# Kernel tuning notes

Hardware: AMD Instinct MI355X
Metric: run time of the kernel (lower is better)

## Reference

```python
import jax, jax.numpy as jnp
import numpy as np

NUM_SLOTS = 7
DIM = 4096
NUM_HEADS = 8
HEAD_DIM = DIM // NUM_HEADS
LN_EPS = 1e-5


def setup_inputs() -> dict:
    key = jax.random.key(0)
    ks = jax.random.split(key, 9)
    B, N = 8, 2048
    x = jax.random.normal(ks[0], (B, N, DIM), dtype=jnp.float32)
    slots = 1e-4 * jax.random.normal(ks[1], (NUM_SLOTS, DIM), dtype=jnp.float32)
    ln_g = jnp.ones((DIM,), jnp.float32)
    ln_b = jnp.zeros((DIM,), jnp.float32)
    # nn.MultiheadAttention packed in-projection: rows [Wq; Wk; Wv], each (DIM, DIM)
    s = 1.0 / np.sqrt(DIM)
    in_proj_w = jax.random.uniform(ks[2], (3 * DIM, DIM), jnp.float32, -s, s)
    in_proj_b = jnp.zeros((3 * DIM,), jnp.float32)
    out_proj_w = jax.random.uniform(ks[3], (DIM, DIM), jnp.float32, -s, s)
    out_proj_b = jnp.zeros((DIM,), jnp.float32)
    alpha = 0.1 * jax.random.normal(ks[4], (1,), jnp.float32)  # nonzero so gate path is active
    return {"x": x, "slots": slots, "ln_g": ln_g, "ln_b": ln_b,
            "in_proj_w": in_proj_w, "in_proj_b": in_proj_b,
            "out_proj_w": out_proj_w, "out_proj_b": out_proj_b, "alpha": alpha}


def _cmrm(x, slots, ln_g, ln_b, in_proj_w, in_proj_b, out_proj_w, out_proj_b, alpha):
    x32 = x.astype(jnp.float32)
    # pre LayerNorm
    mu = jnp.mean(x32, axis=-1, keepdims=True)
    var = jnp.mean(jnp.square(x32 - mu), axis=-1, keepdims=True)
    xn = (x32 - mu) * jax.lax.rsqrt(var + LN_EPS) * ln_g + ln_b  # (B,N,D)
    slots_c = jnp.clip(slots, -10.0, 10.0)  # (Q,D), Q=7
    Wq, Wk, Wv = jnp.split(in_proj_w, 3, axis=0)
    bq, bk, bv = jnp.split(in_proj_b, 3, axis=0)
    q = slots_c @ Wq.T + bq                      # (Q,D), identical for all batches
    k = xn @ Wk.T + bk                           # (B,N,D)
    v = xn @ Wv.T + bv                           # (B,N,D)
    B, N, _ = x.shape
    qh = q.reshape(NUM_SLOTS, NUM_HEADS, HEAD_DIM)          # (Q,H,hd)
    kh = k.reshape(B, N, NUM_HEADS, HEAD_DIM)
    vh = v.reshape(B, N, NUM_HEADS, HEAD_DIM)
    scale = 1.0 / np.sqrt(HEAD_DIM)
    scores = jnp.einsum('qhd,bnhd->bhqn', qh * scale, kh)   # (B,H,Q,N)
    attn = jax.nn.softmax(scores, axis=-1)
    ctx = jnp.einsum('bhqn,bnhd->bqhd', attn, vh).reshape(B, NUM_SLOTS, DIM)
    slots_out = ctx @ out_proj_w.T + out_proj_b             # (B,Q,D)
    slots_res = slots_c[None] + slots_out                   # residual, ungated slots
    gate = jnp.tanh(alpha)                                  # (1,)
    g = jnp.mean(gate * slots_res, axis=1, keepdims=True)   # (B,1,D)
    x_refined = (x32 + g).astype(x.dtype)
    attn_weights = jnp.mean(attn, axis=1)                   # torch avg over heads -> (B,Q,N)
    return x_refined, attn_weights


def reference(x, slots, ln_g, ln_b, in_proj_w, in_proj_b, out_proj_w, out_proj_b, alpha):
    return _cmrm(x, slots, ln_g, ln_b, in_proj_w, in_proj_b, out_proj_w, out_proj_b, alpha)
```

## Files before the change

kernel.cpp:

```cpp
#include <hip/hip_runtime.h>

typedef __attribute__((ext_vector_type(4))) float f32x4;
typedef __attribute__((ext_vector_type(8))) short short8x;

#define DIM   4096
#define NB    8
#define NN    2048
#define NROWS (NB*NN)
#define NHD   8
#define NQ    7
#define NHQ   56
#define SCALE 0.04419417382415922f

#define OFF_MU     0L
#define OFF_RSTD   16384L
#define OFF_Q7     32768L
#define OFF_A      61440L
#define OFF_D0     61504L
#define OFF_S1     61568L
#define OFF_SMST   61632L
#define OFF_CTXM   62528L
#define OFF_GFIN   95296L
#define OFF_YM     128064L
#define OFF_UGBF   390208L
#define OFF_STATP  521280L
#define OFF_SCT    652352L
#define OFF_BIG    1700928L
#define OFF_AM     (OFF_BIG)
#define OFF_PART   (OFF_BIG + 131072L)

__device__ __forceinline__ unsigned short f2bf(float f) {
  union { float f; unsigned int u; } v; v.f = f;
  return (unsigned short)((v.u + 0x7FFFu + ((v.u >> 16) & 1u)) >> 16);
}
__device__ __forceinline__ unsigned short f2bfr(float f) {
  union { float f; unsigned int u; } v; v.f = f;
  return (unsigned short)((v.u + 0x8000u) >> 16);
}

__device__ __forceinline__ float waveSum(float v) {
  #pragma unroll
  for (int m = 1; m < 64; m <<= 1) v += __shfl_xor(v, m);
  return v;
}
__device__ __forceinline__ float blockSum256(float v, float* red) {
  v = waveSum(v);
  __syncthreads();
  if ((threadIdx.x & 63) == 0) red[threadIdx.x >> 6] = v;
  __syncthreads();
  return red[0] + red[1] + red[2] + red[3];
}
__device__ __forceinline__ float blockMax256(float v, float* red) {
  #pragma unroll
  for (int m = 1; m < 64; m <<= 1) v = fmaxf(v, __shfl_xor(v, m));
  __syncthreads();
  if ((threadIdx.x & 63) == 0) red[threadIdx.x >> 6] = v;
  __syncthreads();
  return fmaxf(fmaxf(red[0], red[1]), fmaxf(red[2], red[3]));
}

__global__ __launch_bounds__(256) void k_qproj(const float* __restrict__ ipw,
    const float* __restrict__ ipb, const float* __restrict__ slots, float* __restrict__ q7) {
  const int w = threadIdx.x >> 6, l = threadIdx.x & 63;
  const int d = blockIdx.x * 4 + w;
  const float4* wr4 = (const float4*)(ipw + (long)d * DIM);
  float acc[7] = {0,0,0,0,0,0,0};
  for (int e4 = l; e4 < 1024; e4 += 64) {
    float4 wv = wr4[e4];
    #pragma unroll
    for (int s = 0; s < 7; s++) {
      float4 sv = ((const float4*)(slots + (long)s*DIM))[e4];
      sv.x = fminf(fmaxf(sv.x, -10.f), 10.f); sv.y = fminf(fmaxf(sv.y, -10.f), 10.f);
      sv.z = fminf(fmaxf(sv.z, -10.f), 10.f); sv.w = fminf(fmaxf(sv.w, -10.f), 10.f);
      acc[s] += wv.x*sv.x + wv.y*sv.y + wv.z*sv.z + wv.w*sv.w;
    }
  }
  #pragma unroll
  for (int s = 0; s < 7; s++) acc[s] = waveSum(acc[s]);
  if (l == 0) {
    float bq = ipb[d];
    #pragma unroll
    for (int s = 0; s < 7; s++) q7[(long)s*DIM + d] = acc[s] + bq;
  }
}

__global__ __launch_bounds__(64) void k_adinit(const float* __restrict__ q7,
    const float* __restrict__ ipb, float* __restrict__ Aarr, float* __restrict__ D0arr) {
  const int hq = blockIdx.x, h = hq / 7, q = hq % 7;
  float acc = 0;
  for (int i = threadIdx.x; i < 512; i += 64)
    acc += q7[(long)q*DIM + h*512 + i] * ipb[DIM + h*512 + i];
  acc = waveSum(acc);
  if (threadIdx.x == 0) { Aarr[hq] = 0.f; D0arr[hq] = SCALE * acc; }
}

__global__ __launch_bounds__(256) void k_uproj(const float* __restrict__ ipw,
    const float* __restrict__ q7, float* __restrict__ upart) {
  const int h = blockIdx.y, c = blockIdx.z;
  const int e = blockIdx.x * 256 + threadIdx.x;
  __shared__ float qs[7][128];
  for (int i = threadIdx.x; i < 7*128; i += 256) {
    int s = i >> 7, hd = i & 127;
    qs[s][hd] = q7[(long)s*DIM + h*512 + c*128 + hd];
  }
  __syncthreads();
  float acc[7] = {0,0,0,0,0,0,0};
  const float* wp = ipw + ((long)(DIM + h*512 + c*128))*DIM + e;
  for (int hd = 0; hd < 128; hd++) {
    float wv = wp[(long)hd * DIM];
    #pragma unroll
    for (int s = 0; s < 7; s++) acc[s] += qs[s][hd] * wv;
  }
  #pragma unroll
  for (int s = 0; s < 7; s++) upart[(long)((c*8 + h)*7 + s)*DIM + e] = acc[s];
}

__global__ __launch_bounds__(256) void k_ured(const float* __restrict__ upart,
    const float* __restrict__ lng, const float* __restrict__ lnb,
    unsigned short* __restrict__ ugbf, float* __restrict__ Aarr, float* __restrict__ D0arr) {
  const int h = blockIdx.y;
  const int e = blockIdx.x * 256 + threadIdx.x;
  if (h == 8) {
    #pragma unroll
    for (int r = 0; r < 8; r++) ugbf[(long)(56 + r)*DIM + e] = 0;
    return;
  }
  float ge = lng[e], be = lnb[e];
  #pragma unroll
  for (int s = 0; s < 7; s++) {
    float u = 0;
    #pragma unroll
    for (int c = 0; c < 4; c++) u += upart[(long)((c*8 + h)*7 + s)*DIM + e];
    u *= SCALE;
    ugbf[(long)(h*7 + s)*DIM + e] = f2bf(u * ge);
    float pa = waveSum(u * ge);
    float pd = waveSum(u * be);
    if ((threadIdx.x & 63) == 0) {
      atomicAdd(&Aarr[h*7 + s], pa);
      atomicAdd(&D0arr[h*7 + s], pd);
    }
  }
}

__global__ __launch_bounds__(256) void k_scores2(const float* __restrict__ x,
    const unsigned short* __restrict__ ugbf, float* __restrict__ raw, float2* __restrict__ statp) {
  const int tid = threadIdx.x;
  const int w = tid >> 6, l = tid & 63;
  const int lr = l & 15, lk8 = (l >> 4) * 8;
  const int rowblk = blockIdx.x >> 2, ks = blockIdx.x & 3;
  const int row0w = rowblk * 64 + w * 16;
  const long arow = (long)(row0w + lr) * DIM;
  const int kbase = ks * 1024;
  f32x4 acc0 = {0,0,0,0}, acc1 = {0,0,0,0}, acc2 = {0,0,0,0}, acc3 = {0,0,0,0};
  float sx = 0.f, sxx = 0.f;
  const long b0 = (long)(0*16 + lr)*DIM, b1 = (long)(1*16 + lr)*DIM,
             b2 = (long)(2*16 + lr)*DIM, b3 = (long)(3*16 + lr)*DIM;
  #pragma unroll 2
  for (int kc = kbase; kc < kbase + 1024; kc += 32) {
    const float4 v0 = *(const float4*)(x + arow + kc + lk8);
    const float4 v1 = *(const float4*)(x + arow + kc + lk8 + 4);
    sx  += (v0.x + v0.y) + (v0.z + v0.w) + (v1.x + v1.y) + (v1.z + v1.w);
    sxx += v0.x*v0.x + v0.y*v0.y + v0.z*v0.z + v0.w*v0.w
         + v1.x*v1.x + v1.y*v1.y + v1.z*v1.z + v1.w*v1.w;
    short8x a;
    a[0] = (short)f2bfr(v0.x); a[1] = (short)f2bfr(v0.y);
    a[2] = (short)f2bfr(v0.z); a[3] = (short)f2bfr(v0.w);
    a[4] = (short)f2bfr(v1.x); a[5] = (short)f2bfr(v1.y);
    a[6] = (short)f2bfr(v1.z); a[7] = (short)f2bfr(v1.w);
    short8x bb0 = *(const short8x*)(ugbf + b0 + kc + lk8);
    acc0 = __builtin_amdgcn_mfma_f32_16x16x32_bf16(a, bb0, acc0, 0, 0, 0);
    short8x bb1 = *(const short8x*)(ugbf + b1 + kc + lk8);
    acc1 = __builtin_amdgcn_mfma_f32_16x16x32_bf16(a, bb1, acc1, 0, 0, 0);
    short8x bb2 = *(const short8x*)(ugbf + b2 + kc + lk8);
    acc2 = __builtin_amdgcn_mfma_f32_16x16x32_bf16(a, bb2, acc2, 0, 0, 0);
    short8x bb3 = *(const short8x*)(ugbf + b3 + kc + lk8);
    acc3 = __builtin_amdgcn_mfma_f32_16x16x32_bf16(a, bb3, acc3, 0, 0, 0);
  }
  sx += __shfl_xor(sx, 16);  sx += __shfl_xor(sx, 32);
  sxx += __shfl_xor(sxx, 16); sxx += __shfl_xor(sxx, 32);
  if (l < 16) {
    float2 p; p.x = sx; p.y = sxx;
    statp[(long)ks*NROWS + row0w + l] = p;
  }
  const long base = ((long)ks*NROWS + row0w) * 64;
  #pragma unroll
  for (int i = 0; i < 4; i++) {
    long ro = base + (long)((l >> 4)*4 + i) * 64 + lr;
    raw[ro +  0] = acc0[i];
    raw[ro + 16] = acc1[i];
    raw[ro + 32] = acc2[i];
    raw[ro + 48] = acc3[i];
  }
}

__global__ __launch_bounds__(256) void k_sepi(const float* __restrict__ raw,
    const float2* __restrict__ statp, const float* __restrict__ Aarr,
    const float* __restrict__ D0arr, float* __restrict__ mu_o, float* __restrict__ rstd_o,
    float* __restrict__ sct) {
  const int w = threadIdx.x >> 6, l = threadIdx.x & 63;
  const int row = blockIdx.x * 4 + w;
  float s = 0;
  #pragma unroll
  for (int ks = 0; ks < 4; ks++) s += raw[((long)ks*NROWS + row)*64 + l];
  float sx = 0, sxx = 0;
  #pragma unroll
  for (int ks = 0; ks < 4; ks++) {
    float2 p = statp[(long)ks*NROWS + row];
    sx += p.x; sxx += p.y;
  }
  float mu = sx * (1.0f/DIM), var = sxx * (1.0f/DIM) - mu*mu;
  float rs = rsqrtf(var + 1e-5f);
  if (l == 0) { mu_o[row] = mu; rstd_o[row] = rs; }
  if (l < NHQ) sct[(long)l*NROWS + row] = rs*(s - mu*Aarr[l]) + D0arr[l];
}

__global__ __launch_bounds__(256) void k_smax(const float* __restrict__ sct,
    float2* __restrict__ stats, float* __restrict__ s1) {
  __shared__ float red[4];
  if (blockIdx.x == 0 && threadIdx.x < 64) s1[threadIdx.x] = 0.f;
  const int b = blockIdx.x / NHQ, hq = blockIdx.x % NHQ;
  const int tid = threadIdx.x;
  const float* sp = sct + (long)hq*NROWS + (long)b*NN;
  float s[8]; float mx = -3.4e38f;
  #pragma unroll
  for (int j = 0; j < 8; j++) { s[j] = sp[tid + j*256]; mx = fmaxf(mx, s[j]); }
  mx = blockMax256(mx, red);
  float sum = 0;
  #pragma unroll
  for (int j = 0; j < 8; j++) sum += __expf(s[j] - mx);
  sum = blockSum256(sum, red);
  if (tid == 0) { float2 o; o.x = mx; o.y = 1.0f/sum; stats[b*NHQ + hq] = o; }
}

__global__ __launch_bounds__(256) void k_attnmeans(const float* __restrict__ sct,
    const float2* __restrict__ stats, const float* __restrict__ mu, const float* __restrict__ rstd,
    float* __restrict__ am, float* __restrict__ s1, float* __restrict__ out_attn) {
  const int b = blockIdx.x >> 3, nc = blockIdx.x & 7;
  const int tid = threadIdx.x;
  const int n = nc*256 + tid, row = b*NN + n;
  __shared__ float2 st[56];
  if (tid < 56) st[tid] = stats[b*NHQ + tid];
  __syncthreads();
  const float mur = mu[row] * rstd[row];
  float aq[7] = {0,0,0,0,0,0,0};
  #pragma unroll
  for (int h = 0; h < 8; h++) {
    float ah = 0;
    #pragma unroll
    for (int q = 0; q < 7; q++) {
      float2 s2 = st[h*7 + q];
      float p = __expf(sct[(long)(h*7 + q)*NROWS + row] - s2.x) * s2.y;
      aq[q] += p; ah += p;
    }
    float amv = ah * (1.0f/7.0f);
    am[((long)(b*8 + h))*NN + n] = amv;
    float sv = waveSum(amv * mur);
    if ((tid & 63) == 0) atomicAdd(&s1[b*8 + h], sv);
  }
  #pragma unroll
  for (int q = 0; q < 7; q++) out_attn[((long)(b*NQ + q))*NN + n] = aq[q] * 0.125f;
}

__global__ __launch_bounds__(256) void k_ypart(const float* __restrict__ x,
    const float* __restrict__ am, const float* __restrict__ rstd, float* __restrict__ part) {
  const int bid = blockIdx.x;
  const int b = bid >> 7, ec = (bid >> 5) & 3, nc = bid & 31;
  __shared__ float amr[8][64];
  const int tid = threadIdx.x;
  for (int i = tid; i < 512; i += 256) {
    int h = i >> 6, nn = i & 63;
    int row = b*NN + nc*64 + nn;
    amr[h][nn] = am[((long)(b*8 + h))*NN + nc*64 + nn] * rstd[row];
  }
  __syncthreads();
  const int e = ec*1024 + tid*4;
  float ax[8], ay[8], az[8], aw[8];
  #pragma unroll
  for (int h = 0; h < 8; h++) { ax[h]=0; ay[h]=0; az[h]=0; aw[h]=0; }
  const float* xp = x + ((long)(b*NN + nc*64))*DIM + e;
  #pragma unroll 2
  for (int nn = 0; nn < 64; nn++) {
    const float4 xv = *(const float4*)(xp + (long)nn*DIM);
    #pragma unroll
    for (int h = 0; h < 8; h++) {
      float a = amr[h][nn];
      ax[h] += a*xv.x; ay[h] += a*xv.y; az[h] += a*xv.z; aw[h] += a*xv.w;
    }
  }
  #pragma unroll
  for (int h = 0; h < 8; h++) {
    float4 o; o.x = ax[h]; o.y = ay[h]; o.z = az[h]; o.w = aw[h];
    *(float4*)&part[((long)(nc*64 + b*8 + h))*DIM + e] = o;
  }
}

__global__ __launch_bounds__(256) void k_yred(const float* __restrict__ part,
    const float* __restrict__ s1, const float* __restrict__ lng, const float* __restrict__ lnb,
    float* __restrict__ ym) {
  const long i4 = (long)blockIdx.x*256 + threadIdx.x;
  const float4* p4 = (const float4*)part;
  float4 s = p4[i4];
  #pragma unroll
  for (int nc = 1; nc < 32; nc++) {
    float4 v = p4[(long)nc*65536 + i4];
    s.x += v.x; s.y += v.y; s.z += v.z; s.w += v.w;
  }
  const int bh = (int)(i4 >> 10), e4 = (int)(i4 & 1023);
  float sv = s1[bh];
  float4 g = ((const float4*)lng)[e4], bb = ((const float4*)lnb)[e4];
  float4 o;
  o.x = g.x*(s.x - sv) + bb.x; o.y = g.y*(s.y - sv) + bb.y;
  o.z = g.z*(s.z - sv) + bb.z; o.w = g.w*(s.w - sv) + bb.w;
  ((float4*)ym)[i4] = o;
}

__global__ __launch_bounds__(256) void k_ctxm(const float* __restrict__ ipw,
    const float* __restrict__ ipb, const float* __restrict__ ym, float* __restrict__ ctxm) {
  const int w = threadIdx.x >> 6, l = threadIdx.x & 63;
  const int d = blockIdx.x*4 + w;
  const int h = d >> 9;
  const float4* wr4 = (const float4*)(ipw + ((long)(2*DIM + d))*DIM);
  float acc[8] = {0,0,0,0,0,0,0,0};
  for (int e4 = l; e4 < 1024; e4 += 64) {
    float4 wv = wr4[e4];
    #pragma unroll
    for (int b = 0; b < 8; b++) {
      float4 y = ((const float4*)(ym + (long)(b*8 + h)*DIM))[e4];
      acc[b] += wv.x*y.x + wv.y*y.y + wv.z*y.z + wv.w*y.w;
    }
  }
  #pragma unroll
  for (int b = 0; b < 8; b++) acc[b] = waveSum(acc[b]);
  if (l == 0) {
    float bias = ipb[2*DIM + d];
    #pragma unroll
    for (int b = 0; b < 8; b++) ctxm[(long)b*DIM + d] = acc[b] + bias;
  }
}

__global__ __launch_bounds__(256) void k_gvec(const float* __restrict__ opw,
    const float* __restrict__ opb, const float* __restrict__ ctxm, const float* __restrict__ slots,
    const float* __restrict__ alpha, float* __restrict__ gfin) {
  const int w = threadIdx.x >> 6, l = threadIdx.x & 63;
  const int d = blockIdx.x*4 + w;
  const float4* wr4 = (const float4*)(opw + (long)d*DIM);
  float acc[8] = {0,0,0,0,0,0,0,0};
  for (int e4 = l; e4 < 1024; e4 += 64) {
    float4 wv = wr4[e4];
    #pragma unroll
    for (int b = 0; b < 8; b++) {
      float4 c = ((const float4*)(ctxm + (long)b*DIM))[e4];
      acc[b] += wv.x*c.x + wv.y*c.y + wv.z*c.z + wv.w*c.w;
    }
  }
  #pragma unroll
  for (int b = 0; b < 8; b++) acc[b] = waveSum(acc[b]);
  if (l == 0) {
    float smv = 0;
    #pragma unroll
    for (int q = 0; q < 7; q++)
      smv += fminf(fmaxf(slots[(long)q*DIM + d], -10.f), 10.f);
    smv *= (1.0f/7.0f);
    float t = tanhf(alpha[0]);
    float base = smv + opb[d];
    #pragma unroll
    for (int b = 0; b < 8; b++) gfin[(long)b*DIM + d] = t * (base + acc[b]);
  }
}

__global__ __launch_bounds__(256) void k_refine(const float* __restrict__ x,
    const float* __restrict__ gfin, float* __restrict__ out) {
  const float4* x4 = (const float4*)x;
  const float4* g4 = (const float4*)gfin;
  float4* o4 = (float4*)out;
  const long total = (long)NROWS * 1024;
  for (long i4 = (long)blockIdx.x*256 + threadIdx.x; i4 < total; i4 += (long)gridDim.x*256) {
    long b = i4 >> 21;
    long e4 = i4 & 1023;
    float4 xv = x4[i4], gv = g4[b*1024 + e4];
    float4 o; o.x = xv.x + gv.x; o.y = xv.y + gv.y; o.z = xv.z + gv.z; o.w = xv.w + gv.w;
    o4[i4] = o;
  }
}

extern "C" void kernel_launch(void* const* d_in, const int* in_sizes, int n_in,
                              void* d_out, int out_size, void* d_ws, size_t ws_size,
                              hipStream_t stream) {
  const float* x     = (const float*)d_in[0];
  const float* slots = (const float*)d_in[1];
  const float* lng   = (const float*)d_in[2];
  const float* lnb   = (const float*)d_in[3];
  const float* ipw   = (const float*)d_in[4];
  const float* ipb   = (const float*)d_in[5];
  const float* opw   = (const float*)d_in[6];
  const float* opb   = (const float*)d_in[7];
  const float* alpha = (const float*)d_in[8];
  float* out = (float*)d_out;
  float* ws  = (float*)d_ws;

  float* mu     = ws + OFF_MU;
  float* rstd   = ws + OFF_RSTD;
  float* q7     = ws + OFF_Q7;
  float* Aarr   = ws + OFF_A;
  float* D0arr  = ws + OFF_D0;
  float* s1     = ws + OFF_S1;
  float2* stats = (float2*)(ws + OFF_SMST);
  float* ctxm   = ws + OFF_CTXM;
  float* gfin   = ws + OFF_GFIN;
  float* ym     = ws + OFF_YM;
  unsigned short* ugbf = (unsigned short*)(ws + OFF_UGBF);
  float2* statp = (float2*)(ws + OFF_STATP);
  float* sct    = ws + OFF_SCT;
  float* upart  = ws + OFF_BIG;
  float* raw    = ws + OFF_BIG;
  float* am     = ws + OFF_AM;
  float* part   = ws + OFF_PART;
  float* out_attn = out + (long)NROWS * DIM;

  hipLaunchKernelGGL(k_qproj,     dim3(1024),      dim3(256), 0, stream, ipw, ipb, slots, q7);
  hipLaunchKernelGGL(k_adinit,    dim3(56),        dim3(64),  0, stream, q7, ipb, Aarr, D0arr);
  hipLaunchKernelGGL(k_uproj,     dim3(16, 8, 4),  dim3(256), 0, stream, ipw, q7, upart);
  hipLaunchKernelGGL(k_ured,      dim3(16, 9),     dim3(256), 0, stream, upart, lng, lnb, ugbf, Aarr, D0arr);
  hipLaunchKernelGGL(k_scores2,   dim3(1024),      dim3(256), 0, stream, x, ugbf, raw, statp);
  hipLaunchKernelGGL(k_sepi,      dim3(4096),      dim3(256), 0, stream, raw, statp, Aarr, D0arr, mu, rstd, sct);
  hipLaunchKernelGGL(k_smax,      dim3(448),       dim3(256), 0, stream, sct, stats, s1);
  hipLaunchKernelGGL(k_attnmeans, dim3(64),        dim3(256), 0, stream, sct, stats, mu, rstd, am, s1, out_attn);
  hipLaunchKernelGGL(k_ypart,     dim3(1024),      dim3(256), 0, stream, x, am, rstd, part);
  hipLaunchKernelGGL(k_yred,      dim3(256),       dim3(256), 0, stream, part, s1, lng, lnb, ym);
  hipLaunchKernelGGL(k_ctxm,      dim3(1024),      dim3(256), 0, stream, ipw, ipb, ym, ctxm);
  hipLaunchKernelGGL(k_gvec,      dim3(1024),      dim3(256), 0, stream, opw, opb, ctxm, slots, alpha, gfin);
  hipLaunchKernelGGL(k_refine,    dim3(8192),      dim3(256), 0, stream, x, gfin, out);
}
```

Before: 425.3 us.

## Fuse pipeline stages into persistent megakernel with hierarchical grid barriers

Merges twelve separate kernel launches into one persistent kernel of 512 blocks. The stages are separated by a tree-structured software grid barrier built from atomic counters in the workspace, which is cleared with a memset before launch. Several stages are re-partitioned to match the fixed block count, for example more k-chunks in the u projection and 128-row chunks in ypart. The aim is to remove launch gaps and tail effects between the many small kernels. In exchange it depends on all 512 blocks being co-resident, and the grid-strided stages may leave some CUs with uneven load.

```diff
diff --git a/kernel.cpp b/kernel.cpp
--- a/kernel.cpp
+++ b/kernel.cpp
@@ -7,10 +7,12 @@
 #define NB    8
 #define NN    2048
 #define NROWS (NB*NN)
-#define NHD   8
 #define NQ    7
 #define NHQ   56
 #define SCALE 0.04419417382415922f
+#define NBLKS 512
+#define NLEAF 16
+#define BPL   (NBLKS/NLEAF)
 
 #define OFF_MU     0L
 #define OFF_RSTD   16384L
@@ -18,13 +20,14 @@
 #define OFF_A      61440L
 #define OFF_D0     61504L
 #define OFF_S1     61568L
-#define OFF_SMST   61632L
+#define OFF_SUMEXP 61632L
 #define OFF_CTXM   62528L
 #define OFF_GFIN   95296L
 #define OFF_YM     128064L
 #define OFF_UGBF   390208L
 #define OFF_STATP  521280L
 #define OFF_SCT    652352L
+#define OFF_BAR    1600000L
 #define OFF_BIG    1700928L
 #define OFF_AM     (OFF_BIG)
 #define OFF_PART   (OFF_BIG + 131072L)
@@ -37,334 +40,349 @@
   union { float f; unsigned int u; } v; v.f = f;
   return (unsigned short)((v.u + 0x8000u) >> 16);
 }
-
 __device__ __forceinline__ float waveSum(float v) {
   #pragma unroll
   for (int m = 1; m < 64; m <<= 1) v += __shfl_xor(v, m);
   return v;
 }
-__device__ __forceinline__ float blockSum256(float v, float* red) {
-  v = waveSum(v);
+
+__device__ __forceinline__ void gbar(unsigned* bar, int k) {
   __syncthreads();
-  if ((threadIdx.x & 63) == 0) red[threadIdx.x >> 6] = v;
+  if (threadIdx.x == 0) {
+    __threadfence();
+    unsigned* leaf = bar + 1 + (blockIdx.x & (NLEAF - 1));
+    unsigned a = __hip_atomic_fetch_add(leaf, 1u, __ATOMIC_ACQ_REL, __HIP_MEMORY_SCOPE_AGENT);
+    if (a == (unsigned)((k + 1) * BPL - 1)) {
+      unsigned r = __hip_atomic_fetch_add(bar + 17, 1u, __ATOMIC_ACQ_REL, __HIP_MEMORY_SCOPE_AGENT);
+      if (r == (unsigned)((k + 1) * NLEAF - 1))
+        __hip_atomic_fetch_add(bar, 1u, __ATOMIC_ACQ_REL, __HIP_MEMORY_SCOPE_AGENT);
+    }
+    while (__hip_atomic_load(bar, __ATOMIC_ACQUIRE, __HIP_MEMORY_SCOPE_AGENT) < (unsigned)(k + 1))
+      __builtin_amdgcn_s_sleep(8);
+    __threadfence();
+  }
   __syncthreads();
-  return red[0] + red[1] + red[2] + red[3];
-}
-__device__ __forceinline__ float blockMax256(float v, float* red) {
-  #pragma unroll
-  for (int m = 1; m < 64; m <<= 1) v = fmaxf(v, __shfl_xor(v, m));
-  __syncthreads();
-  if ((threadIdx.x & 63) == 0) red[threadIdx.x >> 6] = v;
-  __syncthreads();
-  return fmaxf(fmaxf(red[0], red[1]), fmaxf(red[2], red[3]));
-}
-
-__global__ __launch_bounds__(256) void k_qproj(const float* __restrict__ ipw,
-    const float* __restrict__ ipb, const float* __restrict__ slots, float* __restrict__ q7) {
-  const int w = threadIdx.x >> 6, l = threadIdx.x & 63;
-  const int d = blockIdx.x * 4 + w;
-  const float4* wr4 = (const float4*)(ipw + (long)d * DIM);
-  float acc[7] = {0,0,0,0,0,0,0};
-  for (int e4 = l; e4 < 1024; e4 += 64) {
-    float4 wv = wr4[e4];
+}
+
+__global__ __launch_bounds__(256, 4) void k_mega(
+    const float* __restrict__ x, const float* __restrict__ slots,
+    const float* __restrict__ lng, const float* __restrict__ lnb,
+    const float* __restrict__ ipw, const float* __restrict__ ipb,
+    const float* __restrict__ opw, const float* __restrict__ opb,
+    const float* __restrict__ alpha, float* __restrict__ out, float* __restrict__ ws) {
+  __shared__ float smem[1024];
+  const int bid = blockIdx.x, tid = threadIdx.x;
+  const int w = tid >> 6, l = tid & 63;
+
+  float* mu     = ws + OFF_MU;
+  float* rstd   = ws + OFF_RSTD;
+  float* q7     = ws + OFF_Q7;
+  float* Aarr   = ws + OFF_A;
+  float* D0arr  = ws + OFF_D0;
+  float* s1     = ws + OFF_S1;
+  float* sumexp = ws + OFF_SUMEXP;
+  float* ctxm   = ws + OFF_CTXM;
+  float* gfin   = ws + OFF_GFIN;
+  float* ym     = ws + OFF_YM;
+  unsigned short* ugbf = (unsigned short*)(ws + OFF_UGBF);
+  float2* statp = (float2*)(ws + OFF_STATP);
+  float* sct    = ws + OFF_SCT;
+  unsigned* bar = (unsigned*)(ws + OFF_BAR);
+  float* upart  = ws + OFF_BIG;
+  float* raw    = ws + OFF_BIG;
+  float* am     = ws + OFF_AM;
+  float* part   = ws + OFF_PART;
+  float* out_attn = out + (long)NROWS * DIM;
+
+  if (bid == 0) {
+    if (tid < 448) sumexp[tid] = 0.f;
+    else if (tid < 512) s1[tid - 448] = 0.f;
+  } else if (bid <= 8) {
+    unsigned* u32 = (unsigned*)ugbf;
+    const long r = 56 + bid - 1;
+    #pragma unroll
+    for (int j = 0; j < 8; j++) u32[r*2048 + (long)tid*8 + j] = 0u;
+  }
+  for (int vb = bid; vb < 1024; vb += NBLKS) {
+    const int d = vb * 4 + w;
+    const float4* wr4 = (const float4*)(ipw + (long)d * DIM);
+    float acc[7] = {0,0,0,0,0,0,0};
+    for (int e4 = l; e4 < 1024; e4 += 64) {
+      float4 wv = wr4[e4];
+      #pragma unroll
+      for (int s = 0; s < 7; s++) {
+        float4 sv = ((const float4*)(slots + (long)s*DIM))[e4];
+        sv.x = fminf(fmaxf(sv.x, -10.f), 10.f); sv.y = fminf(fmaxf(sv.y, -10.f), 10.f);
+        sv.z = fminf(fmaxf(sv.z, -10.f), 10.f); sv.w = fminf(fmaxf(sv.w, -10.f), 10.f);
+        acc[s] += wv.x*sv.x + wv.y*sv.y + wv.z*sv.z + wv.w*sv.w;
+      }
+    }
+    #pragma unroll
+    for (int s = 0; s < 7; s++) acc[s] = waveSum(acc[s]);
+    if (l == 0) {
+      float bq = ipb[d];
+      #pragma unroll
+      for (int s = 0; s < 7; s++) q7[(long)s*DIM + d] = acc[s] + bq;
+    }
+  }
+  gbar(bar, 0);
+
+  if (bid < 14) {
+    const int hq = bid * 4 + w;
+    if (hq < NHQ) {
+      const int h = hq / 7, q = hq % 7;
+      float acc = 0;
+      for (int i = l; i < 512; i += 64)
+        acc += q7[(long)q*DIM + h*512 + i] * ipb[DIM + h*512 + i];
+      acc = waveSum(acc);
+      if (l == 0) { Aarr[hq] = 0.f; D0arr[hq] = SCALE * acc; }
+    }
+  }
+  {
+    const int bx = bid & 3, h = (bid >> 2) & 7, c = bid >> 5;
+    if (tid < 224) {
+      int s = tid >> 5, hd = tid & 31;
+      smem[tid] = q7[(long)s*DIM + h*512 + c*32 + hd];
+    }
+    __syncthreads();
+    const int e0 = bx*1024 + tid*4;
+    float4 acc[7];
+    #pragma unroll
+    for (int s = 0; s < 7; s++) { acc[s].x = 0; acc[s].y = 0; acc[s].z = 0; acc[s].w = 0; }
+    #pragma unroll 4
+    for (int hd = 0; hd < 32; hd++) {
+      float4 wv = *(const float4*)(ipw + ((long)(DIM + h*512 + c*32 + hd))*DIM + e0);
+      #pragma unroll
+      for (int s = 0; s < 7; s++) {
+        float qv = smem[s*32 + hd];
+        acc[s].x += qv*wv.x; acc[s].y += qv*wv.y; acc[s].z += qv*wv.z; acc[s].w += qv*wv.w;
+      }
+    }
+    #pragma unroll
+    for (int s = 0; s < 7; s++)
+      *(float4*)&upart[(long)((c*8 + h)*7 + s)*DIM + e0] = acc[s];
+  }
+  gbar(bar, 1);
+
+  if (bid < 128) {
+    const int bx = bid & 15, h = bid >> 4;
+    const int e = bx*256 + tid;
+    float ge = lng[e], be = lnb[e];
     #pragma unroll
     for (int s = 0; s < 7; s++) {
-      float4 sv = ((const float4*)(slots + (long)s*DIM))[e4];
-      sv.x = fminf(fmaxf(sv.x, -10.f), 10.f); sv.y = fminf(fmaxf(sv.y, -10.f), 10.f);
-      sv.z = fminf(fmaxf(sv.z, -10.f), 10.f); sv.w = fminf(fmaxf(sv.w, -10.f), 10.f);
-      acc[s] += wv.x*sv.x + wv.y*sv.y + wv.z*sv.z + wv.w*sv.w;
-    }
-  }
-  #pragma unroll
-  for (int s = 0; s < 7; s++) acc[s] = waveSum(acc[s]);
-  if (l == 0) {
-    float bq = ipb[d];
-    #pragma unroll
-    for (int s = 0; s < 7; s++) q7[(long)s*DIM + d] = acc[s] + bq;
-  }
-}
-
-__global__ __launch_bounds__(64) void k_adinit(const float* __restrict__ q7,
-    const float* __restrict__ ipb, float* __restrict__ Aarr, float* __restrict__ D0arr) {
-  const int hq = blockIdx.x, h = hq / 7, q = hq % 7;
-  float acc = 0;
-  for (int i = threadIdx.x; i < 512; i += 64)
-    acc += q7[(long)q*DIM + h*512 + i] * ipb[DIM + h*512 + i];
-  acc = waveSum(acc);
-  if (threadIdx.x == 0) { Aarr[hq] = 0.f; D0arr[hq] = SCALE * acc; }
-}
-
-__global__ __launch_bounds__(256) void k_uproj(const float* __restrict__ ipw,
-    const float* __restrict__ q7, float* __restrict__ upart) {
-  const int h = blockIdx.y, c = blockIdx.z;
-  const int e = blockIdx.x * 256 + threadIdx.x;
-  __shared__ float qs[7][128];
-  for (int i = threadIdx.x; i < 7*128; i += 256) {
-    int s = i >> 7, hd = i & 127;
-    qs[s][hd] = q7[(long)s*DIM + h*512 + c*128 + hd];
-  }
-  __syncthreads();
-  float acc[7] = {0,0,0,0,0,0,0};
-  const float* wp = ipw + ((long)(DIM + h*512 + c*128))*DIM + e;
-  for (int hd = 0; hd < 128; hd++) {
-    float wv = wp[(long)hd * DIM];
-    #pragma unroll
-    for (int s = 0; s < 7; s++) acc[s] += qs[s][hd] * wv;
-  }
-  #pragma unroll
-  for (int s = 0; s < 7; s++) upart[(long)((c*8 + h)*7 + s)*DIM + e] = acc[s];
-}
-
-__global__ __launch_bounds__(256) void k_ured(const float* __restrict__ upart,
-    const float* __restrict__ lng, const float* __restrict__ lnb,
-    unsigned short* __restrict__ ugbf, float* __restrict__ Aarr, float* __restrict__ D0arr) {
-  const int h = blockIdx.y;
-  const int e = blockIdx.x * 256 + threadIdx.x;
-  if (h == 8) {
-    #pragma unroll
-    for (int r = 0; r < 8; r++) ugbf[(long)(56 + r)*DIM + e] = 0;
-    return;
-  }
-  float ge = lng[e], be = lnb[e];
-  #pragma unroll
-  for (int s = 0; s < 7; s++) {
-    float u = 0;
-    #pragma unroll
-    for (int c = 0; c < 4; c++) u += upart[(long)((c*8 + h)*7 + s)*DIM + e];
-    u *= SCALE;
-    ugbf[(long)(h*7 + s)*DIM + e] = f2bf(u * ge);
-    float pa = waveSum(u * ge);
-    float pd = waveSum(u * be);
-    if ((threadIdx.x & 63) == 0) {
-      atomicAdd(&Aarr[h*7 + s], pa);
-      atomicAdd(&D0arr[h*7 + s], pd);
-    }
-  }
-}
-
-__global__ __launch_bounds__(256) void k_scores2(const float* __restrict__ x,
-    const unsigned short* __restrict__ ugbf, float* __restrict__ raw, float2* __restrict__ statp) {
-  const int tid = threadIdx.x;
-  const int w = tid >> 6, l = tid & 63;
-  const int lr = l & 15, lk8 = (l >> 4) * 8;
-  const int rowblk = blockIdx.x >> 2, ks = blockIdx.x & 3;
-  const int row0w = rowblk * 64 + w * 16;
-  const long arow = (long)(row0w + lr) * DIM;
-  const int kbase = ks * 1024;
-  f32x4 acc0 = {0,0,0,0}, acc1 = {0,0,0,0}, acc2 = {0,0,0,0}, acc3 = {0,0,0,0};
-  float sx = 0.f, sxx = 0.f;
-  const long b0 = (long)(0*16 + lr)*DIM, b1 = (long)(1*16 + lr)*DIM,
-             b2 = (long)(2*16 + lr)*DIM, b3 = (long)(3*16 + lr)*DIM;
-  #pragma unroll 2
-  for (int kc = kbase; kc < kbase + 1024; kc += 32) {
-    const float4 v0 = *(const float4*)(x + arow + kc + lk8);
-    const float4 v1 = *(const float4*)(x + arow + kc + lk8 + 4);
-    sx  += (v0.x + v0.y) + (v0.z + v0.w) + (v1.x + v1.y) + (v1.z + v1.w);
-    sxx += v0.x*v0.x + v0.y*v0.y + v0.z*v0.z + v0.w*v0.w
-         + v1.x*v1.x + v1.y*v1.y + v1.z*v1.z + v1.w*v1.w;
-    short8x a;
-    a[0] = (short)f2bfr(v0.x); a[1] = (short)f2bfr(v0.y);
-    a[2] = (short)f2bfr(v0.z); a[3] = (short)f2bfr(v0.w);
-    a[4] = (short)f2bfr(v1.x); a[5] = (short)f2bfr(v1.y);
-    a[6] = (short)f2bfr(v1.z); a[7] = (short)f2bfr(v1.w);
-    short8x bb0 = *(const short8x*)(ugbf + b0 + kc + lk8);
-    acc0 = __builtin_amdgcn_mfma_f32_16x16x32_bf16(a, bb0, acc0, 0, 0, 0);
-    short8x bb1 = *(const short8x*)(ugbf + b1 + kc + lk8);
-    acc1 = __builtin_amdgcn_mfma_f32_16x16x32_bf16(a, bb1, acc1, 0, 0, 0);
-    short8x bb2 = *(const short8x*)(ugbf + b2 + kc + lk8);
-    acc2 = __builtin_amdgcn_mfma_f32_16x16x32_bf16(a, bb2, acc2, 0, 0, 0);
-    short8x bb3 = *(const short8x*)(ugbf + b3 + kc + lk8);
-    acc3 = __builtin_amdgcn_mfma_f32_16x16x32_bf16(a, bb3, acc3, 0, 0, 0);
-  }
-  sx += __shfl_xor(sx, 16);  sx += __shfl_xor(sx, 32);
-  sxx += __shfl_xor(sxx, 16); sxx += __shfl_xor(sxx, 32);
-  if (l < 16) {
-    float2 p; p.x = sx; p.y = sxx;
-    statp[(long)ks*NROWS + row0w + l] = p;
-  }
-  const long base = ((long)ks*NROWS + row0w) * 64;
-  #pragma unroll
-  for (int i = 0; i < 4; i++) {
-    long ro = base + (long)((l >> 4)*4 + i) * 64 + lr;
-    raw[ro +  0] = acc0[i];
-    raw[ro + 16] = acc1[i];
-    raw[ro + 32] = acc2[i];
-    raw[ro + 48] = acc3[i];
-  }
-}
-
-__global__ __launch_bounds__(256) void k_sepi(const float* __restrict__ raw,
-    const float2* __restrict__ statp, const float* __restrict__ Aarr,
-    const float* __restrict__ D0arr, float* __restrict__ mu_o, float* __restrict__ rstd_o,
-    float* __restrict__ sct) {
-  const int w = threadIdx.x >> 6, l = threadIdx.x & 63;
-  const int row = blockIdx.x * 4 + w;
-  float s = 0;
-  #pragma unroll
-  for (int ks = 0; ks < 4; ks++) s += raw[((long)ks*NROWS + row)*64 + l];
-  float sx = 0, sxx = 0;
-  #pragma unroll
-  for (int ks = 0; ks < 4; ks++) {
-    float2 p = statp[(long)ks*NROWS + row];
-    sx += p.x; sxx += p.y;
-  }
-  float mu = sx * (1.0f/DIM), var = sxx * (1.0f/DIM) - mu*mu;
-  float rs = rsqrtf(var + 1e-5f);
-  if (l == 0) { mu_o[row] = mu; rstd_o[row] = rs; }
-  if (l < NHQ) sct[(long)l*NROWS + row] = rs*(s - mu*Aarr[l]) + D0arr[l];
-}
-
-__global__ __launch_bounds__(256) void k_smax(const float* __restrict__ sct,
-    float2* __restrict__ stats, float* __restrict__ s1) {
-  __shared__ float red[4];
-  if (blockIdx.x == 0 && threadIdx.x < 64) s1[threadIdx.x] = 0.f;
-  const int b = blockIdx.x / NHQ, hq = blockIdx.x % NHQ;
-  const int tid = threadIdx.x;
-  const float* sp = sct + (long)hq*NROWS + (long)b*NN;
-  float s[8]; float mx = -3.4e38f;
-  #pragma unroll
-  for (int j = 0; j < 8; j++) { s[j] = sp[tid + j*256]; mx = fmaxf(mx, s[j]); }
-  mx = blockMax256(mx, red);
-  float sum = 0;
-  #pragma unroll
-  for (int j = 0; j < 8; j++) sum += __expf(s[j] - mx);
-  sum = blockSum256(sum, red);
-  if (tid == 0) { float2 o; o.x = mx; o.y = 1.0f/sum; stats[b*NHQ + hq] = o; }
-}
-
-__global__ __launch_bounds__(256) void k_attnmeans(const float* __restrict__ sct,
-    const float2* __restrict__ stats, const float* __restrict__ mu, const float* __restrict__ rstd,
-    float* __restrict__ am, float* __restrict__ s1, float* __restrict__ out_attn) {
-  const int b = blockIdx.x >> 3, nc = blockIdx.x & 7;
-  const int tid = threadIdx.x;
-  const int n = nc*256 + tid, row = b*NN + n;
-  __shared__ float2 st[56];
-  if (tid < 56) st[tid] = stats[b*NHQ + tid];
-  __syncthreads();
-  const float mur = mu[row] * rstd[row];
-  float aq[7] = {0,0,0,0,0,0,0};
-  #pragma unroll
-  for (int h = 0; h < 8; h++) {
-    float ah = 0;
-    #pragma unroll
-    for (int q = 0; q < 7; q++) {
-      float2 s2 = st[h*7 + q];
-      float p = __expf(sct[(long)(h*7 + q)*NROWS + row] - s2.x) * s2.y;
-      aq[q] += p; ah += p;
-    }
-    float amv = ah * (1.0f/7.0f);
-    am[((long)(b*8 + h))*NN + n] = amv;
-    float sv = waveSum(amv * mur);
-    if ((tid & 63) == 0) atomicAdd(&s1[b*8 + h], sv);
-  }
-  #pragma unroll
-  for (int q = 0; q < 7; q++) out_attn[((long)(b*NQ + q))*NN + n] = aq[q] * 0.125f;
-}
-
-__global__ __launch_bounds__(256) void k_ypart(const float* __restrict__ x,
-    const float* __restrict__ am, const float* __restrict__ rstd, float* __restrict__ part) {
-  const int bid = blockIdx.x;
-  const int b = bid >> 7, ec = (bid >> 5) & 3, nc = bid & 31;
-  __shared__ float amr[8][64];
-  const int tid = threadIdx.x;
-  for (int i = tid; i < 512; i += 256) {
-    int h = i >> 6, nn = i & 63;
-    int row = b*NN + nc*64 + nn;
-    amr[h][nn] = am[((long)(b*8 + h))*NN + nc*64 + nn] * rstd[row];
-  }
-  __syncthreads();
-  const int e = ec*1024 + tid*4;
-  float ax[8], ay[8], az[8], aw[8];
-  #pragma unroll
-  for (int h = 0; h < 8; h++) { ax[h]=0; ay[h]=0; az[h]=0; aw[h]=0; }
-  const float* xp = x + ((long)(b*NN + nc*64))*DIM + e;
-  #pragma unroll 2
-  for (int nn = 0; nn < 64; nn++) {
-    const float4 xv = *(const float4*)(xp + (long)nn*DIM);
+      float u = 0;
+      #pragma unroll
+      for (int c = 0; c < 16; c++) u += upart[(long)((c*8 + h)*7 + s)*DIM + e];
+      u *= SCALE;
+      ugbf[(long)(h*7 + s)*DIM + e] = f2bf(u * ge);
+      float pa = waveSum(u * ge);
+      float pd = waveSum(u * be);
+      if (l == 0) {
+        atomicAdd(&Aarr[h*7 + s], pa);
+        atomicAdd(&D0arr[h*7 + s], pd);
+      }
+    }
+  }
+  gbar(bar, 2);
+
+  for (int vb = bid; vb < 1024; vb += NBLKS) {
+    const int lr = l & 15, lk8 = (l >> 4) * 8;
+    const int rowblk = vb >> 2, ks = vb & 3;
+    const int row0w = rowblk * 64 + w * 16;
+    const long arow = (long)(row0w + lr) * DIM;
+    const int kbase = ks * 1024;
+    f32x4 acc0 = {0,0,0,0}, acc1 = {0,0,0,0}, acc2 = {0,0,0,0}, acc3 = {0,0,0,0};
+    float sx = 0.f, sxx = 0.f;
+    const long b0 = (long)(0*16 + lr)*DIM, b1 = (long)(1*16 + lr)*DIM,
+               b2 = (long)(2*16 + lr)*DIM, b3 = (long)(3*16 + lr)*DIM;
+    #pragma unroll 2
+    for (int kc = kbase; kc < kbase + 1024; kc += 32) {
+      const float4 v0 = *(const float4*)(x + arow + kc + lk8);
+      const float4 v1 = *(const float4*)(x + arow + kc + lk8 + 4);
+      sx  += (v0.x + v0.y) + (v0.z + v0.w) + (v1.x + v1.y) + (v1.z + v1.w);
+      sxx += v0.x*v0.x + v0.y*v0.y + v0.z*v0.z + v0.w*v0.w
+           + v1.x*v1.x + v1.y*v1.y + v1.z*v1.z + v1.w*v1.w;
+      short8x a;
+      a[0] = (short)f2bfr(v0.x); a[1] = (short)f2bfr(v0.y);
+      a[2] = (short)f2bfr(v0.z); a[3] = (short)f2bfr(v0.w);
+      a[4] = (short)f2bfr(v1.x); a[5] = (short)f2bfr(v1.y);
+      a[6] = (short)f2bfr(v1.z); a[7] = (short)f2bfr(v1.w);
+      short8x bb0 = *(const short8x*)(ugbf + b0 + kc + lk8);
+      acc0 = __builtin_amdgcn_mfma_f32_16x16x32_bf16(a, bb0, acc0, 0, 0, 0);
+      short8x bb1 = *(const short8x*)(ugbf + b1 + kc + lk8);
+      acc1 = __builtin_amdgcn_mfma_f32_16x16x32_bf16(a, bb1, acc1, 0, 0, 0);
+      short8x bb2 = *(const short8x*)(ugbf + b2 + kc + lk8);
+      acc2 = __builtin_amdgcn_mfma_f32_16x16x32_bf16(a, bb2, acc2, 0, 0, 0);
+      short8x bb3 = *(const short8x*)(ugbf + b3 + kc + lk8);
+      acc3 = __builtin_amdgcn_mfma_f32_16x16x32_bf16(a, bb3, acc3, 0, 0, 0);
+    }
+    sx += __shfl_xor(sx, 16);  sx += __shfl_xor(sx, 32);
+    sxx += __shfl_xor(sxx, 16); sxx += __shfl_xor(sxx, 32);
+    if (l < 16) {
+      float2 p; p.x = sx; p.y = sxx;
+      statp[(long)ks*NROWS + row0w + l] = p;
+    }
+    const long base = ((long)ks*NROWS + row0w) * 64;
+    #pragma unroll
+    for (int i = 0; i < 4; i++) {
+      long ro = base + (long)((l >> 4)*4 + i) * 64 + lr;
+      raw[ro +  0] = acc0[i];
+      raw[ro + 16] = acc1[i];
+      raw[ro + 32] = acc2[i];
+      raw[ro + 48] = acc3[i];
+    }
+  }
+  gbar(bar, 3);
+
+  for (int vb = bid; vb < 1024; vb += NBLKS) {
+    const int b = vb >> 7;
+    float esum = 0.f;
+    #pragma unroll
+    for (int r4 = 0; r4 < 4; r4++) {
+      const int row = vb*16 + w*4 + r4;
+      float s = 0;
+      #pragma unroll
+      for (int ks = 0; ks < 4; ks++) s += raw[((long)ks*NROWS + row)*64 + l];
+      float sx = 0, sxx = 0;
+      #pragma unroll
+      for (int ks = 0; ks < 4; ks++) {
+        float2 p = statp[(long)ks*NROWS + row];
+        sx += p.x; sxx += p.y;
+      }
+      float muv = sx * (1.0f/DIM), var = sxx * (1.0f/DIM) - muv*muv;
+      float rs = rsqrtf(var + 1e-5f);
+      if (l == 0) { mu[row] = muv; rstd[row] = rs; }
+      if (l < NHQ) {
+        float e = __expf(rs*(s - muv*Aarr[l]) + D0arr[l]);
+        sct[(long)l*NROWS + row] = e;
+        esum += e;
+      }
+    }
+    __syncthreads();
+    smem[w*64 + l] = esum;
+    __syncthreads();
+    if (w == 0 && l < NHQ) {
+      float tot = smem[l] + smem[64 + l] + smem[128 + l] + smem[192 + l];
+      atomicAdd(&sumexp[b*NHQ + l], tot);
+    }
+    __syncthreads();
+  }
+  gbar(bar, 4);
+
+  if (bid < 64) {
+    const int b = bid >> 3, nc = bid & 7;
+    const int n = nc*256 + tid, row = b*NN + n;
+    if (tid < NHQ) smem[tid] = 1.0f / sumexp[b*NHQ + tid];
+    __syncthreads();
+    const float mur = mu[row] * rstd[row];
+    float aq[7] = {0,0,0,0,0,0,0};
     #pragma unroll
     for (int h = 0; h < 8; h++) {
-      float a = amr[h][nn];
-      ax[h] += a*xv.x; ay[h] += a*xv.y; az[h] += a*xv.z; aw[h] += a*xv.w;
-    }
-  }
-  #pragma unroll
-  for (int h = 0; h < 8; h++) {
-    float4 o; o.x = ax[h]; o.y = ay[h]; o.z = az[h]; o.w = aw[h];
-    *(float4*)&part[((long)(nc*64 + b*8 + h))*DIM + e] = o;
-  }
-}
-
-__global__ __launch_bounds__(256) void k_yred(const float* __restrict__ part,
-    const float* __restrict__ s1, const float* __restrict__ lng, const float* __restrict__ lnb,
-    float* __restrict__ ym) {
-  const long i4 = (long)blockIdx.x*256 + threadIdx.x;
-  const float4* p4 = (const float4*)part;
-  float4 s = p4[i4];
-  #pragma unroll
-  for (int nc = 1; nc < 32; nc++) {
-    float4 v = p4[(long)nc*65536 + i4];
-    s.x += v.x; s.y += v.y; s.z += v.z; s.w += v.w;
-  }
-  const int bh = (int)(i4 >> 10), e4 = (int)(i4 & 1023);
-  float sv = s1[bh];
-  float4 g = ((const float4*)lng)[e4], bb = ((const float4*)lnb)[e4];
-  float4 o;
-  o.x = g.x*(s.x - sv) + bb.x; o.y = g.y*(s.y - sv) + bb.y;
-  o.z = g.z*(s.z - sv) + bb.z; o.w = g.w*(s.w - sv) + bb.w;
-  ((float4*)ym)[i4] = o;
-}
-
-__global__ __launch_bounds__(256) void k_ctxm(const float* __restrict__ ipw,
-    const float* __restrict__ ipb, const float* __restrict__ ym, float* __restrict__ ctxm) {
-  const int w = threadIdx.x >> 6, l = threadIdx.x & 63;
-  const int d = blockIdx.x*4 + w;
-  const int h = d >> 9;
-  const float4* wr4 = (const float4*)(ipw + ((long)(2*DIM + d))*DIM);
-  float acc[8] = {0,0,0,0,0,0,0,0};
-  for (int e4 = l; e4 < 1024; e4 += 64) {
-    float4 wv = wr4[e4];
-    #pragma unroll
-    for (int b = 0; b < 8; b++) {
-      float4 y = ((const float4*)(ym + (long)(b*8 + h)*DIM))[e4];
-      acc[b] += wv.x*y.x + wv.y*y.y + wv.z*y.z + wv.w*y.w;
-    }
-  }
-  #pragma unroll
-  for (int b = 0; b < 8; b++) acc[b] = waveSum(acc[b]);
-  if (l == 0) {
-    float bias = ipb[2*DIM + d];
-    #pragma unroll
-    for (int b = 0; b < 8; b++) ctxm[(long)b*DIM + d] = acc[b] + bias;
-  }
-}
-
-__global__ __launch_bounds__(256) void k_gvec(const float* __restrict__ opw,
-    const float* __restrict__ opb, const float* __restrict__ ctxm, const float* __restrict__ slots,
-    const float* __restrict__ alpha, float* __restrict__ gfin) {
-  const int w = threadIdx.x >> 6, l = threadIdx.x & 63;
-  const int d = blockIdx.x*4 + w;
-  const float4* wr4 = (const float4*)(opw + (long)d*DIM);
-  float acc[8] = {0,0,0,0,0,0,0,0};
-  for (int e4 = l; e4 < 1024; e4 += 64) {
-    float4 wv = wr4[e4];
-    #pragma unroll
-    for (int b = 0; b < 8; b++) {
-      float4 c = ((const float4*)(ctxm + (long)b*DIM))[e4];
-      acc[b] += wv.x*c.x + wv.y*c.y + wv.z*c.z + wv.w*c.w;
-    }
-  }
-  #pragma unroll
-  for (int b = 0; b < 8; b++) acc[b] = waveSum(acc[b]);
-  if (l == 0) {
-    float smv = 0;
-    #pragma unroll
-    for (int q = 0; q < 7; q++)
-      smv += fminf(fmaxf(slots[(long)q*DIM + d], -10.f), 10.f);
-    smv *= (1.0f/7.0f);
-    float t = tanhf(alpha[0]);
-    float base = smv + opb[d];
-    #pragma unroll
-    for (int b = 0; b < 8; b++) gfin[(long)b*DIM + d] = t * (base + acc[b]);
+      float ah = 0;
+      #pragma unroll
+      for (int q = 0; q < 7; q++) {
+        float p = sct[(long)(h*7 + q)*NROWS + row] * smem[h*7 + q];
+        aq[q] += p; ah += p;
+      }
+      float amv = ah * (1.0f/7.0f);
+      am[((long)(b*8 + h))*NN + n] = amv;
+      float sv = waveSum(amv * mur);
+      if (l == 0) atomicAdd(&s1[b*8 + h], sv);
+    }
+    #pragma unroll
+    for (int q = 0; q < 7; q++) out_attn[((long)(b*NQ + q))*NN + n] = aq[q] * 0.125f;
+  }
+  gbar(bar, 5);
+
+  {
+    const int b = bid >> 6, ec = (bid >> 4) & 3, nc = bid & 15;
+    for (int i = tid; i < 1024; i += 256) {
+      int h = i >> 7, nn = i & 127;
+      int row = b*NN + nc*128 + nn;
+      smem[h*128 + nn] = am[((long)(b*8 + h))*NN + nc*128 + nn] * rstd[row];
+    }
+    __syncthreads();
+    const int e = ec*1024 + tid*4;
+    float ax[8], ay[8], az[8], aw[8];
+    #pragma unroll
+    for (int h = 0; h < 8; h++) { ax[h]=0; ay[h]=0; az[h]=0; aw[h]=0; }
+    const float* xp = x + ((long)(b*NN + nc*128))*DIM + e;
+    #pragma unroll 2
+    for (int nn = 0; nn < 128; nn++) {
+      const float4 xv = *(const float4*)(xp + (long)nn*DIM);
+      #pragma unroll
+      for (int h = 0; h < 8; h++) {
+        float a = smem[h*128 + nn];
+        ax[h] += a*xv.x; ay[h] += a*xv.y; az[h] += a*xv.z; aw[h] += a*xv.w;
+      }
+    }
+    #pragma unroll
+    for (int h = 0; h < 8; h++) {
+      float4 o; o.x = ax[h]; o.y = ay[h]; o.z = az[h]; o.w = aw[h];
+      *(float4*)&part[((long)(nc*64 + b*8 + h))*DIM + e] = o;
+    }
+    __syncthreads();
+  }
+  gbar(bar, 6);
+
+  for (int it = 0; it < 2; it++) {
+    const int i = it*131072 + bid*256 + tid;
+    float s = 0;
+    #pragma unroll
+    for (int nc = 0; nc < 16; nc++) s += part[(long)nc*262144 + i];
+    const int bh = i >> 12, e = i & 4095;
+    ym[i] = lng[e]*(s - s1[bh]) + lnb[e];
+  }
+  gbar(bar, 7);
+
+  for (int vb = bid; vb < 1024; vb += NBLKS) {
+    const int d = vb*4 + w;
+    const int h = d >> 9;
+    const float4* wr4 = (const float4*)(ipw + ((long)(2*DIM + d))*DIM);
+    float acc[8] = {0,0,0,0,0,0,0,0};
+    for (int e4 = l; e4 < 1024; e4 += 64) {
+      float4 wv = wr4[e4];
+      #pragma unroll
+      for (int b = 0; b < 8; b++) {
+        float4 y = ((const float4*)(ym + (long)(b*8 + h)*DIM))[e4];
+        acc[b] += wv.x*y.x + wv.y*y.y + wv.z*y.z + wv.w*y.w;
+      }
+    }
+    #pragma unroll
+    for (int b = 0; b < 8; b++) acc[b] = waveSum(acc[b]);
+    if (l == 0) {
+      float bias = ipb[2*DIM + d];
+      #pragma unroll
+      for (int b = 0; b < 8; b++) ctxm[(long)b*DIM + d] = acc[b] + bias;
+    }
+  }
+  gbar(bar, 8);
+
+  for (int vb = bid; vb < 1024; vb += NBLKS) {
+    const int d = vb*4 + w;
+    const float4* wr4 = (const float4*)(opw + (long)d*DIM);
+    float acc[8] = {0,0,0,0,0,0,0,0};
+    for (int e4 = l; e4 < 1024; e4 += 64) {
+      float4 wv = wr4[e4];
+      #pragma unroll
+      for (int b = 0; b < 8; b++) {
+        float4 c = ((const float4*)(ctxm + (long)b*DIM))[e4];
+        acc[b] += wv.x*c.x + wv.y*c.y + wv.z*c.z + wv.w*c.w;
+      }
+    }
+    #pragma unroll
+    for (int b = 0; b < 8; b++) acc[b] = waveSum(acc[b]);
+    if (l == 0) {
+      float smv = 0;
+      #pragma unroll
+      for (int q = 0; q < 7; q++)
+        smv += fminf(fmaxf(slots[(long)q*DIM + d], -10.f), 10.f);
+      smv *= (1.0f/7.0f);
+      float t = tanhf(alpha[0]);
+      float base = smv + opb[d];
+      #pragma unroll
+      for (int b = 0; b < 8; b++) gfin[(long)b*DIM + d] = t * (base + acc[b]);
+    }
   }
 }
 
@@ -398,36 +416,10 @@
   float* out = (float*)d_out;
   float* ws  = (float*)d_ws;
 
-  float* mu     = ws + OFF_MU;
-  float* rstd   = ws + OFF_RSTD;
-  float* q7     = ws + OFF_Q7;
-  float* Aarr   = ws + OFF_A;
-  float* D0arr  = ws + OFF_D0;
-  float* s1     = ws + OFF_S1;
-  float2* stats = (float2*)(ws + OFF_SMST);
-  float* ctxm   = ws + OFF_CTXM;
-  float* gfin   = ws + OFF_GFIN;
-  float* ym     = ws + OFF_YM;
-  unsigned short* ugbf = (unsigned short*)(ws + OFF_UGBF);
-  float2* statp = (float2*)(ws + OFF_STATP);
-  float* sct    = ws + OFF_SCT;
-  float* upart  = ws + OFF_BIG;
-  float* raw    = ws + OFF_BIG;
-  float* am     = ws + OFF_AM;
-  float* part   = ws + OFF_PART;
-  float* out_attn = out + (long)NROWS * DIM;
-
-  hipLaunchKernelGGL(k_qproj,     dim3(1024),      dim3(256), 0, stream, ipw, ipb, slots, q7);
-  hipLaunchKernelGGL(k_adinit,    dim3(56),        dim3(64),  0, stream, q7, ipb, Aarr, D0arr);
-  hipLaunchKernelGGL(k_uproj,     dim3(16, 8, 4),  dim3(256), 0, stream, ipw, q7, upart);
-  hipLaunchKernelGGL(k_ured,      dim3(16, 9),     dim3(256), 0, stream, upart, lng, lnb, ugbf, Aarr, D0arr);
-  hipLaunchKernelGGL(k_scores2,   dim3(1024),      dim3(256), 0, stream, x, ugbf, raw, statp);
-  hipLaunchKernelGGL(k_sepi,      dim3(4096),      dim3(256), 0, stream, raw, statp, Aarr, D0arr, mu, rstd, sct);
-  hipLaunchKernelGGL(k_smax,      dim3(448),       dim3(256), 0, stream, sct, stats, s1);
-  hipLaunchKernelGGL(k_attnmeans, dim3(64),        dim3(256), 0, stream, sct, stats, mu, rstd, am, s1, out_attn);
-  hipLaunchKernelGGL(k_ypart,     dim3(1024),      dim3(256), 0, stream, x, am, rstd, part);
-  hipLaunchKernelGGL(k_yred,      dim3(256),       dim3(256), 0, stream, part, s1, lng, lnb, ym);
-  hipLaunchKernelGGL(k_ctxm,      dim3(1024),      dim3(256), 0, stream, ipw, ipb, ym, ctxm);
-  hipLaunchKernelGGL(k_gvec,      dim3(1024),      dim3(256), 0, stream, opw, opb, ctxm, slots, alpha, gfin);
-  hipLaunchKernelGGL(k_refine,    dim3(8192),      dim3(256), 0, stream, x, gfin, out);
-}
+  hipMemsetAsync((char*)d_ws + OFF_BAR*4, 0, 128, stream);
+
+  hipLaunchKernelGGL(k_mega, dim3(NBLKS), dim3(256), 0, stream,
+                     x, slots, lng, lnb, ipw, ipb, opw, opb, alpha, out, ws);
+  hipLaunchKernelGGL(k_refine, dim3(8192), dim3(256), 0, stream,
+                     x, ws + OFF_GFIN, out);
+}
```

Result: slower. 1.197 ms (+181.4%).
